# Performance work log

Measured on AMD Instinct MI355X. Metric: run time of the kernel, lower is better.

Reference implementation:

```python
import jax, jax.numpy as jnp
import numpy as np
import math

B, S, D = 4, 2048, 768
H = 12
DH = D // H  # 64
NEG = -1e10

def setup_inputs() -> dict:
    key = jax.random.key(0)
    ks = jax.random.split(key, 8)
    scale = 0.02
    return {
        "hidden_states": jax.random.normal(ks[0], (B, S, D), dtype=jnp.float32),
        "attention_mask": jnp.zeros((B, 1, 1, S), dtype=jnp.float32),
        "Wq": jax.random.normal(ks[1], (D, D), dtype=jnp.float32) * scale,
        "bq": jnp.zeros((D,), dtype=jnp.float32),
        "Wk": jax.random.normal(ks[2], (D, D), dtype=jnp.float32) * scale,
        "bk": jnp.zeros((D,), dtype=jnp.float32),
        "Wv": jax.random.normal(ks[3], (D, D), dtype=jnp.float32) * scale,
        "bv": jnp.zeros((D,), dtype=jnp.float32),
    }

def reference(hidden_states, attention_mask, Wq, bq, Wk, bk, Wv, bv):
    # Linear projections; note attention_mask is accepted but unused, matching the torch module.
    def split_heads(x):  # [B,S,D] -> [B,H,S,DH]
        return x.reshape(B, S, H, DH).transpose(0, 2, 1, 3)
    q = split_heads(hidden_states @ Wq + bq)
    k = split_heads(hidden_states @ Wk + bk)
    v = split_heads(hidden_states @ Wv + bv)
    scores = jnp.einsum("bhqd,bhkd->bhqk", q, k) / math.sqrt(DH)
    causal = jnp.tril(jnp.ones((S, S), dtype=bool))  # masked_fill(mask==0, -1e10)
    scores = jnp.where(causal, scores, NEG)
    probs = jax.nn.softmax(scores, axis=-1)
    # dropout prob = 0.0 (eval) -> identity
    ctx = jnp.einsum("bhqk,bhkd->bhqd", probs, v)
    return ctx.transpose(0, 2, 1, 3).reshape(B, S, D)
```

## Files before the change

kernel.cpp:

```cpp
#include <hip/hip_runtime.h>
#include <hip/hip_bf16.h>

#define B_  4
#define S_  2048
#define D_  768
#define H_  12
#define DH_ 64

typedef __bf16 bf16;
typedef __attribute__((ext_vector_type(8))) __bf16 bf16x8;
typedef __attribute__((ext_vector_type(4))) __bf16 bf16x4;
typedef __attribute__((ext_vector_type(4))) float floatx4;

__device__ __forceinline__ int chunk_off(int qt) {
    if (qt < 8)  return qt;
    if (qt < 16) return 8 + 2 * (qt - 8);
    if (qt < 24) return 24 + 3 * (qt - 16);
    return 48 + 4 * (qt - 24);
}

__global__ __launch_bounds__(256) void cvt_f32_bf16(const float* __restrict__ in,
                                                    bf16* __restrict__ out, int n4) {
    int i = blockIdx.x * 256 + threadIdx.x;
    if (i < n4) {
        float4 v = ((const float4*)in)[i];
        bf16x4 o;
        o[0] = (bf16)v.x; o[1] = (bf16)v.y; o[2] = (bf16)v.z; o[3] = (bf16)v.w;
        *(bf16x4*)(out + (size_t)i * 4) = o;
    }
}

__global__ __launch_bounds__(256) void w_transpose(const float* __restrict__ w0,
                                                   const float* __restrict__ w1,
                                                   const float* __restrict__ w2,
                                                   bf16* __restrict__ Wt)
{
    const int which = blockIdx.z;
    const float* W = (which == 0) ? w0 : (which == 1 ? w1 : w2);
    bf16* dst = Wt + (size_t)which * D_ * D_;
    __shared__ bf16 t[64 * 72];
    const int k0 = blockIdx.x * 64, n0 = blockIdx.y * 64;
    const int tid = threadIdx.x;
    {
        int r = tid >> 2;
        int c0 = (tid & 3) * 16;
        #pragma unroll
        for (int q = 0; q < 4; q++) {
            float4 v = *(const float4*)(W + (size_t)(k0 + r) * D_ + n0 + c0 + q * 4);
            t[(c0 + q * 4 + 0) * 72 + r] = (bf16)v.x;
            t[(c0 + q * 4 + 1) * 72 + r] = (bf16)v.y;
            t[(c0 + q * 4 + 2) * 72 + r] = (bf16)v.z;
            t[(c0 + q * 4 + 3) * 72 + r] = (bf16)v.w;
        }
    }
    __syncthreads();
    {
        int n = tid >> 3, seg = tid & 7;
        *(bf16x8*)(dst + (size_t)(n0 + n) * D_ + k0 + seg * 8) =
            *(const bf16x8*)(t + n * 72 + seg * 8);
        *(bf16x8*)(dst + (size_t)(n0 + n + 32) * D_ + k0 + seg * 8) =
            *(const bf16x8*)(t + (n + 32) * 72 + seg * 8);
    }
}

__global__ __launch_bounds__(256) void qkv_gemm(
    const bf16* __restrict__ Xb, const bf16* __restrict__ Wt,
    const float* __restrict__ bq, const float* __restrict__ bk,
    const float* __restrict__ bv, bf16* __restrict__ QKV)
{
    const int which = blockIdx.z;
    const bf16* Wm = Wt + (size_t)which * D_ * D_;
    const float* bias = (which == 0) ? bq : (which == 1 ? bk : bv);
    bf16* out = QKV + (size_t)which * B_ * H_ * S_ * DH_;

    __shared__ bf16 As[128 * 72];
    __shared__ bf16 Bs[128 * 72];

    const int tid  = threadIdx.x;
    const int wave = tid >> 6, lane = tid & 63;
    const int wr = wave >> 1, wc = wave & 1;
    const int g = lane >> 4, ln = lane & 15;
    const int m0 = blockIdx.x * 128, n0 = blockIdx.y * 128;

    floatx4 acc[4][4];
    #pragma unroll
    for (int i = 0; i < 4; i++)
        #pragma unroll
        for (int j = 0; j < 4; j++)
            acc[i][j] = (floatx4){0.f, 0.f, 0.f, 0.f};

    int row_[4], seg_[4];
    #pragma unroll
    for (int t = 0; t < 4; t++) { int fc = tid + t * 256; row_[t] = fc >> 3; seg_[t] = fc & 7; }

    bf16x8 apf[4], bpf[4];
    #pragma unroll
    for (int t = 0; t < 4; t++) {
        apf[t] = *(const bf16x8*)(Xb + (size_t)(m0 + row_[t]) * D_ + seg_[t] * 8);
        bpf[t] = *(const bf16x8*)(Wm + (size_t)(n0 + row_[t]) * D_ + seg_[t] * 8);
    }

    for (int k0 = 0; k0 < D_; k0 += 64) {
        __syncthreads();
        #pragma unroll
        for (int t = 0; t < 4; t++) {
            *(bf16x8*)(As + row_[t] * 72 + seg_[t] * 8) = apf[t];
            *(bf16x8*)(Bs + row_[t] * 72 + seg_[t] * 8) = bpf[t];
        }
        __syncthreads();
        if (k0 + 64 < D_) {
            #pragma unroll
            for (int t = 0; t < 4; t++) {
                apf[t] = *(const bf16x8*)(Xb + (size_t)(m0 + row_[t]) * D_ + k0 + 64 + seg_[t] * 8);
                bpf[t] = *(const bf16x8*)(Wm + (size_t)(n0 + row_[t]) * D_ + k0 + 64 + seg_[t] * 8);
            }
        }
        #pragma unroll
        for (int ks = 0; ks < 2; ks++) {
            bf16x8 af[4], bfr[4];
            #pragma unroll
            for (int i = 0; i < 4; i++)
                af[i] = *(const bf16x8*)(As + (wr * 64 + i * 16 + ln) * 72 + ks * 32 + g * 8);
            #pragma unroll
            for (int j = 0; j < 4; j++)
                bfr[j] = *(const bf16x8*)(Bs + (wc * 64 + j * 16 + ln) * 72 + ks * 32 + g * 8);
            #pragma unroll
            for (int i = 0; i < 4; i++)
                #pragma unroll
                for (int j = 0; j < 4; j++)
                    acc[i][j] = __builtin_amdgcn_mfma_f32_16x16x32_bf16(af[i], bfr[j], acc[i][j], 0, 0, 0);
        }
    }

    #pragma unroll
    for (int i = 0; i < 4; i++) {
        #pragma unroll
        for (int j = 0; j < 4; j++) {
            int col = n0 + wc * 64 + j * 16 + ln;
            float bv_ = bias[col];
            int h = col >> 6, dh = col & 63;
            int rowbase = m0 + wr * 64 + i * 16 + g * 4;
            int b = rowbase >> 11, s0 = rowbase & 2047;
            if (which == 2) {
                bf16x4 o;
                #pragma unroll
                for (int r = 0; r < 4; r++) o[r] = (bf16)(acc[i][j][r] + bv_);
                *(bf16x4*)(out + ((size_t)((b * H_ + h) * DH_ + dh)) * S_ + s0) = o;
            } else {
                #pragma unroll
                for (int r = 0; r < 4; r++)
                    out[(((size_t)(b * H_ + h) * S_ + s0 + r) << 6) + dh] =
                        (bf16)(acc[i][j][r] + bv_);
            }
        }
    }
}

__global__ __launch_bounds__(256) void attn_chunk(const bf16* __restrict__ QKV,
                                                  float* __restrict__ out,
                                                  bf16* __restrict__ Opart,
                                                  float* __restrict__ Lpart)
{
    const int cid = 79 - blockIdx.x;
    const int bh = blockIdx.y;
    const int b = bh / H_, h = bh % H_;

    int qt, c;
    if (cid < 8)       { qt = cid; c = 0; }
    else if (cid < 24) { qt = 8 + ((cid - 8) >> 1); c = (cid - 8) & 1; }
    else if (cid < 48) { int t3 = cid - 24; qt = 16 + t3 / 3; c = t3 - (qt - 16) * 3; }
    else               { int t4 = cid - 48; qt = 24 + (t4 >> 2); c = t4 & 3; }
    const int nch = (qt >> 3) + 1;
    const int kt0 = c * 8;
    const int kt1 = min(kt0 + 7, qt);

    const size_t MAT = (size_t)B_ * H_ * S_ * DH_;
    const bf16* Q  = QKV +           (size_t)bh * S_ * DH_;
    const bf16* K  = QKV + MAT +     (size_t)bh * S_ * DH_;
    const bf16* Vt = QKV + 2 * MAT + (size_t)bh * S_ * DH_;

    __shared__ bf16 Ks[64 * 72];
    __shared__ bf16 Vts[64 * 72];
    __shared__ bf16 Ps[4][16 * 72];

    const int tid  = threadIdx.x;
    const int wave = tid >> 6, lane = tid & 63;
    const int g = lane >> 4, ln = lane & 15;
    const int srow = tid >> 3, sseg = tid & 7;

    bf16x8 qf[2];
    {
        const bf16* qrow = Q + (size_t)(qt * 64 + wave * 16 + ln) * DH_;
        qf[0] = *(const bf16x8*)(qrow + g * 8);
        qf[1] = *(const bf16x8*)(qrow + 32 + g * 8);
    }

    bf16x8 ones;
    #pragma unroll
    for (int i = 0; i < 8; i++) ones[i] = (bf16)1.0f;

    floatx4 accO[4];
    #pragma unroll
    for (int j = 0; j < 4; j++) accO[j] = (floatx4){0.f, 0.f, 0.f, 0.f};
    floatx4 accL = (floatx4){0.f, 0.f, 0.f, 0.f};

    const bf16* kptr = K  + (size_t)(kt0 * 64 + srow) * DH_ + sseg * 8;
    const bf16* vptr = Vt + (size_t)srow * S_ + kt0 * 64 + sseg * 8;

    bf16x8 ka = *(const bf16x8*)kptr;
    bf16x8 kb = *(const bf16x8*)(kptr + 32 * DH_);
    bf16x8 va = *(const bf16x8*)vptr;
    bf16x8 vb = *(const bf16x8*)(vptr + (size_t)32 * S_);

    for (int kt = kt0; kt <= kt1; ++kt) {
        __syncthreads();
        *(bf16x8*)(Ks  + srow * 72 + sseg * 8) = ka;
        *(bf16x8*)(Ks  + (srow + 32) * 72 + sseg * 8) = kb;
        *(bf16x8*)(Vts + srow * 72 + sseg * 8) = va;
        *(bf16x8*)(Vts + (srow + 32) * 72 + sseg * 8) = vb;
        __syncthreads();
        if (kt < kt1) {
            kptr += 64 * DH_;
            vptr += 64;
            ka = *(const bf16x8*)kptr;
            kb = *(const bf16x8*)(kptr + 32 * DH_);
            va = *(const bf16x8*)vptr;
            vb = *(const bf16x8*)(vptr + (size_t)32 * S_);
        }

        floatx4 accS[4];
        #pragma unroll
        for (int j = 0; j < 4; j++) accS[j] = (floatx4){0.f, 0.f, 0.f, 0.f};
        #pragma unroll
        for (int j = 0; j < 4; j++) {
            #pragma unroll
            for (int cc = 0; cc < 2; cc++) {
                bf16x8 kf = *(const bf16x8*)(Ks + (j * 16 + ln) * 72 + cc * 32 + g * 8);
                accS[j] = __builtin_amdgcn_mfma_f32_16x16x32_bf16(qf[cc], kf, accS[j], 0, 0, 0);
            }
        }

        #pragma unroll
        for (int j = 0; j < 4; j++)
            #pragma unroll
            for (int r = 0; r < 4; r++)
                accS[j][r] = __expf(accS[j][r] * 0.125f);
        if (kt == qt) {
            #pragma unroll
            for (int j = 0; j < 4; j++) {
                int krow = j * 16 + ln;
                #pragma unroll
                for (int r = 0; r < 4; r++) {
                    int qrow = wave * 16 + g * 4 + r;
                    if (krow > qrow) accS[j][r] = 0.f;
                }
            }
        }

        bf16* Pw = Ps[wave];
        #pragma unroll
        for (int j = 0; j < 4; j++)
            #pragma unroll
            for (int r = 0; r < 4; r++)
                Pw[(g * 4 + r) * 72 + j * 16 + ln] = (bf16)accS[j][r];

        #pragma unroll
        for (int cc = 0; cc < 2; cc++) {
            bf16x8 pf = *(const bf16x8*)(Pw + ln * 72 + cc * 32 + g * 8);
            accL = __builtin_amdgcn_mfma_f32_16x16x32_bf16(pf, ones, accL, 0, 0, 0);
            #pragma unroll
            for (int j = 0; j < 4; j++) {
                bf16x8 vf = *(const bf16x8*)(Vts + (j * 16 + ln) * 72 + cc * 32 + g * 8);
                accO[j] = __builtin_amdgcn_mfma_f32_16x16x32_bf16(pf, vf, accO[j], 0, 0, 0);
            }
        }
    }

    if (nch == 1) {
        float inv[4];
        #pragma unroll
        for (int r = 0; r < 4; r++) inv[r] = 1.0f / accL[r];
        #pragma unroll
        for (int j = 0; j < 4; j++) {
            int dh = j * 16 + ln;
            #pragma unroll
            for (int r = 0; r < 4; r++) {
                int q = qt * 64 + wave * 16 + g * 4 + r;
                out[((size_t)(b * S_ + q)) * D_ + h * DH_ + dh] = accO[j][r] * inv[r];
            }
        }
    } else {
        const int chunk = bh * 80 + chunk_off(qt) + c;
        bf16x8 p0, p1;
        #pragma unroll
        for (int e = 0; e < 8; e++) {
            p0[e] = (bf16)accO[e >> 2][e & 3];
            p1[e] = (bf16)accO[2 + (e >> 2)][e & 3];
        }
        bf16* dst = Opart + (size_t)chunk * 4096 + tid * 16;
        *(bf16x8*)dst = p0;
        *(bf16x8*)(dst + 8) = p1;
        if (ln == 0) {
            #pragma unroll
            for (int r = 0; r < 4; r++)
                Lpart[chunk * 64 + wave * 16 + g * 4 + r] = accL[r];
        }
    }
}

__global__ __launch_bounds__(256) void attn_reduce(const bf16* __restrict__ Opart,
                                                   const float* __restrict__ Lpart,
                                                   float* __restrict__ out)
{
    const int qt = 8 + blockIdx.x;
    const int bh = blockIdx.y;
    const int b = bh / H_, h = bh % H_;
    const int nch = (qt >> 3) + 1;
    const int cb = bh * 80 + chunk_off(qt);

    const int tid  = threadIdx.x;
    const int wave = tid >> 6, lane = tid & 63;
    const int g = lane >> 4, ln = lane & 15;

    float o[16];
    #pragma unroll
    for (int e = 0; e < 16; e++) o[e] = 0.f;
    float ls[4] = {0.f, 0.f, 0.f, 0.f};

    for (int cidx = 0; cidx < nch; cidx++) {
        const bf16* p = Opart + (size_t)(cb + cidx) * 4096 + tid * 16;
        bf16x8 v0 = *(const bf16x8*)p;
        bf16x8 v1 = *(const bf16x8*)(p + 8);
        #pragma unroll
        for (int e = 0; e < 8; e++) { o[e] += (float)v0[e]; o[8 + e] += (float)v1[e]; }
        #pragma unroll
        for (int r = 0; r < 4; r++)
            ls[r] += Lpart[(cb + cidx) * 64 + wave * 16 + g * 4 + r];
    }
    float inv[4];
    #pragma unroll
    for (int r = 0; r < 4; r++) inv[r] = 1.0f / ls[r];
    #pragma unroll
    for (int j = 0; j < 4; j++) {
        int dh = j * 16 + ln;
        #pragma unroll
        for (int r = 0; r < 4; r++) {
            int q = qt * 64 + wave * 16 + g * 4 + r;
            out[((size_t)(b * S_ + q)) * D_ + h * DH_ + dh] = o[j * 4 + r] * inv[r];
        }
    }
}

extern "C" void kernel_launch(void* const* d_in, const int* in_sizes, int n_in,
                              void* d_out, int out_size, void* d_ws, size_t ws_size,
                              hipStream_t stream) {
    const float* hs = (const float*)d_in[0];
    const float* Wq = (const float*)d_in[2];
    const float* bq = (const float*)d_in[3];
    const float* Wk = (const float*)d_in[4];
    const float* bk = (const float*)d_in[5];
    const float* Wv = (const float*)d_in[6];
    const float* bv = (const float*)d_in[7];
    float* out = (float*)d_out;

    bf16* Xb    = (bf16*)d_ws;
    bf16* Wt    = Xb + (size_t)8192 * 768;
    bf16* QKV   = Wt + (size_t)3 * 768 * 768;
    bf16* Opart = QKV + (size_t)3 * B_ * H_ * S_ * DH_;
    float* Lpart = (float*)(Opart + (size_t)3840 * 4096);

    cvt_f32_bf16<<<6144, 256, 0, stream>>>(hs, Xb, 1572864);
    w_transpose<<<dim3(12, 12, 3), 256, 0, stream>>>(Wq, Wk, Wv, Wt);
    qkv_gemm<<<dim3(64, 6, 3), 256, 0, stream>>>(Xb, Wt, bq, bk, bv, QKV);
    attn_chunk<<<dim3(80, 48), 256, 0, stream>>>(QKV, out, Opart, Lpart);
    attn_reduce<<<dim3(24, 48), 256, 0, stream>>>(Opart, Lpart, out);
}
```

Baseline: 202.1 us.

## Process two query tiles per attention block and transpose P via shuffles

```diff
diff --git a/kernel.cpp b/kernel.cpp
--- a/kernel.cpp
+++ b/kernel.cpp
@@ -12,11 +12,17 @@
 typedef __attribute__((ext_vector_type(4))) __bf16 bf16x4;
 typedef __attribute__((ext_vector_type(4))) float floatx4;
 
-__device__ __forceinline__ int chunk_off(int qt) {
-    if (qt < 8)  return qt;
-    if (qt < 16) return 8 + 2 * (qt - 8);
-    if (qt < 24) return 24 + 3 * (qt - 16);
-    return 48 + 4 * (qt - 24);
+__device__ __forceinline__ int chunk_off2(int qt2) {
+    if (qt2 < 4)  return qt2;
+    if (qt2 < 8)  return 4 + 2 * (qt2 - 4);
+    if (qt2 < 12) return 12 + 3 * (qt2 - 8);
+    return 24 + 4 * (qt2 - 12);
+}
+
+__device__ __forceinline__ unsigned pack_bf16(float a, float b) {
+    unsigned short ua = __builtin_bit_cast(unsigned short, (bf16)a);
+    unsigned short ub = __builtin_bit_cast(unsigned short, (bf16)b);
+    return (unsigned)ua | ((unsigned)ub << 16);
 }
 
 __global__ __launch_bounds__(256) void cvt_f32_bf16(const float* __restrict__ in,
@@ -132,6 +138,7 @@
         }
     }
 
+    const float sc = (which == 0) ? 0.125f : 1.0f;
     #pragma unroll
     for (int i = 0; i < 4; i++) {
         #pragma unroll
@@ -150,7 +157,7 @@
                 #pragma unroll
                 for (int r = 0; r < 4; r++)
                     out[(((size_t)(b * H_ + h) * S_ + s0 + r) << 6) + dh] =
-                        (bf16)(acc[i][j][r] + bv_);
+                        (bf16)((acc[i][j][r] + bv_) * sc);
             }
         }
     }
@@ -161,18 +168,18 @@
                                                   bf16* __restrict__ Opart,
                                                   float* __restrict__ Lpart)
 {
-    const int cid = 79 - blockIdx.x;
+    const int cid = 39 - blockIdx.x;
     const int bh = blockIdx.y;
     const int b = bh / H_, h = bh % H_;
 
-    int qt, c;
-    if (cid < 8)       { qt = cid; c = 0; }
-    else if (cid < 24) { qt = 8 + ((cid - 8) >> 1); c = (cid - 8) & 1; }
-    else if (cid < 48) { int t3 = cid - 24; qt = 16 + t3 / 3; c = t3 - (qt - 16) * 3; }
-    else               { int t4 = cid - 48; qt = 24 + (t4 >> 2); c = t4 & 3; }
-    const int nch = (qt >> 3) + 1;
+    int qt2, c;
+    if (cid < 4)       { qt2 = cid; c = 0; }
+    else if (cid < 12) { int t = cid - 4;  qt2 = 4 + (t >> 1);  c = t & 1; }
+    else if (cid < 24) { int t = cid - 12; qt2 = 8 + t / 3;     c = t - 3 * (t / 3); }
+    else               { int t = cid - 24; qt2 = 12 + (t >> 2); c = t & 3; }
+    const int nch = (2 * qt2 + 9) >> 3;
     const int kt0 = c * 8;
-    const int kt1 = min(kt0 + 7, qt);
+    const int kt1 = min(kt0 + 7, 2 * qt2 + 1);
 
     const size_t MAT = (size_t)B_ * H_ * S_ * DH_;
     const bf16* Q  = QKV +           (size_t)bh * S_ * DH_;
@@ -181,36 +188,41 @@
 
     __shared__ bf16 Ks[64 * 72];
     __shared__ bf16 Vts[64 * 72];
-    __shared__ bf16 Ps[4][16 * 72];
 
     const int tid  = threadIdx.x;
     const int wave = tid >> 6, lane = tid & 63;
     const int g = lane >> 4, ln = lane & 15;
     const int srow = tid >> 3, sseg = tid & 7;
-
-    bf16x8 qf[2];
-    {
-        const bf16* qrow = Q + (size_t)(qt * 64 + wave * 16 + ln) * DH_;
-        qf[0] = *(const bf16x8*)(qrow + g * 8);
-        qf[1] = *(const bf16x8*)(qrow + 32 + g * 8);
+    const int qbase = qt2 * 128;
+
+    bf16x8 qf[2][2];
+    #pragma unroll
+    for (int t = 0; t < 2; t++) {
+        const bf16* qrow = Q + (size_t)(qbase + t * 64 + wave * 16 + ln) * DH_;
+        qf[t][0] = *(const bf16x8*)(qrow + g * 8);
+        qf[t][1] = *(const bf16x8*)(qrow + 32 + g * 8);
     }
 
     bf16x8 ones;
     #pragma unroll
     for (int i = 0; i < 8; i++) ones[i] = (bf16)1.0f;
 
-    floatx4 accO[4];
-    #pragma unroll
-    for (int j = 0; j < 4; j++) accO[j] = (floatx4){0.f, 0.f, 0.f, 0.f};
-    floatx4 accL = (floatx4){0.f, 0.f, 0.f, 0.f};
+    floatx4 accO[2][4];
+    #pragma unroll
+    for (int t = 0; t < 2; t++)
+        #pragma unroll
+        for (int j = 0; j < 4; j++) accO[t][j] = (floatx4){0.f, 0.f, 0.f, 0.f};
+    floatx4 accL[2] = {(floatx4){0.f, 0.f, 0.f, 0.f}, (floatx4){0.f, 0.f, 0.f, 0.f}};
 
     const bf16* kptr = K  + (size_t)(kt0 * 64 + srow) * DH_ + sseg * 8;
     const bf16* vptr = Vt + (size_t)srow * S_ + kt0 * 64 + sseg * 8;
-
     bf16x8 ka = *(const bf16x8*)kptr;
     bf16x8 kb = *(const bf16x8*)(kptr + 32 * DH_);
     bf16x8 va = *(const bf16x8*)vptr;
     bf16x8 vb = *(const bf16x8*)(vptr + (size_t)32 * S_);
+
+    const int s0lane = ((lane >> 4) & 1) * 32 + ln;
+    const bool hi = (lane >= 32);
 
     for (int kt = kt0; kt <= kt1; ++kt) {
         __syncthreads();
@@ -228,82 +240,108 @@
             vb = *(const bf16x8*)(vptr + (size_t)32 * S_);
         }
 
-        floatx4 accS[4];
-        #pragma unroll
-        for (int j = 0; j < 4; j++) accS[j] = (floatx4){0.f, 0.f, 0.f, 0.f};
-        #pragma unroll
-        for (int j = 0; j < 4; j++) {
-            #pragma unroll
-            for (int cc = 0; cc < 2; cc++) {
-                bf16x8 kf = *(const bf16x8*)(Ks + (j * 16 + ln) * 72 + cc * 32 + g * 8);
-                accS[j] = __builtin_amdgcn_mfma_f32_16x16x32_bf16(qf[cc], kf, accS[j], 0, 0, 0);
-            }
-        }
-
+        bf16x8 kf[4][2];
         #pragma unroll
         for (int j = 0; j < 4; j++)
             #pragma unroll
-            for (int r = 0; r < 4; r++)
-                accS[j][r] = __expf(accS[j][r] * 0.125f);
-        if (kt == qt) {
+            for (int cc = 0; cc < 2; cc++)
+                kf[j][cc] = *(const bf16x8*)(Ks + (j * 16 + ln) * 72 + cc * 32 + g * 8);
+
+        floatx4 accS[2][4];
+        #pragma unroll
+        for (int t = 0; t < 2; t++)
+            #pragma unroll
+            for (int j = 0; j < 4; j++) accS[t][j] = (floatx4){0.f, 0.f, 0.f, 0.f};
+        #pragma unroll
+        for (int t = 0; t < 2; t++)
+            #pragma unroll
+            for (int j = 0; j < 4; j++)
+                #pragma unroll
+                for (int cc = 0; cc < 2; cc++)
+                    accS[t][j] = __builtin_amdgcn_mfma_f32_16x16x32_bf16(
+                        kf[j][cc], qf[t][cc], accS[t][j], 0, 0, 0);
+
+        unsigned pd0[2][4], pd1[2][4];
+        #pragma unroll
+        for (int t = 0; t < 2; t++) {
+            const int qg = qbase + t * 64 + wave * 16 + ln;
+            const bool domask = (kt >= 2 * qt2 + t);
             #pragma unroll
             for (int j = 0; j < 4; j++) {
-                int krow = j * 16 + ln;
+                float p[4];
                 #pragma unroll
                 for (int r = 0; r < 4; r++) {
-                    int qrow = wave * 16 + g * 4 + r;
-                    if (krow > qrow) accS[j][r] = 0.f;
+                    p[r] = __expf(accS[t][j][r]);
+                    if (domask) {
+                        int key = kt * 64 + j * 16 + g * 4 + r;
+                        if (key > qg) p[r] = 0.f;
+                    }
                 }
-            }
-        }
-
-        bf16* Pw = Ps[wave];
-        #pragma unroll
-        for (int j = 0; j < 4; j++)
-            #pragma unroll
-            for (int r = 0; r < 4; r++)
-                Pw[(g * 4 + r) * 72 + j * 16 + ln] = (bf16)accS[j][r];
+                pd0[t][j] = pack_bf16(p[0], p[1]);
+                pd1[t][j] = pack_bf16(p[2], p[3]);
+            }
+        }
 
         #pragma unroll
         for (int cc = 0; cc < 2; cc++) {
-            bf16x8 pf = *(const bf16x8*)(Pw + ln * 72 + cc * 32 + g * 8);
-            accL = __builtin_amdgcn_mfma_f32_16x16x32_bf16(pf, ones, accL, 0, 0, 0);
+            bf16x8 ptf[2];
+            #pragma unroll
+            for (int t = 0; t < 2; t++) {
+                unsigned a0 = __shfl(pd0[t][2 * cc],     s0lane);
+                unsigned b0 = __shfl(pd0[t][2 * cc + 1], s0lane);
+                unsigned a1 = __shfl(pd1[t][2 * cc],     s0lane);
+                unsigned b1 = __shfl(pd1[t][2 * cc + 1], s0lane);
+                unsigned a2 = __shfl(pd0[t][2 * cc],     s0lane + 16);
+                unsigned b2 = __shfl(pd0[t][2 * cc + 1], s0lane + 16);
+                unsigned a3 = __shfl(pd1[t][2 * cc],     s0lane + 16);
+                unsigned b3 = __shfl(pd1[t][2 * cc + 1], s0lane + 16);
+                uint4 w;
+                w.x = hi ? b0 : a0;
+                w.y = hi ? b1 : a1;
+                w.z = hi ? b2 : a2;
+                w.w = hi ? b3 : a3;
+                ptf[t] = __builtin_bit_cast(bf16x8, w);
+                accL[t] = __builtin_amdgcn_mfma_f32_16x16x32_bf16(ones, ptf[t], accL[t], 0, 0, 0);
+            }
             #pragma unroll
             for (int j = 0; j < 4; j++) {
                 bf16x8 vf = *(const bf16x8*)(Vts + (j * 16 + ln) * 72 + cc * 32 + g * 8);
-                accO[j] = __builtin_amdgcn_mfma_f32_16x16x32_bf16(pf, vf, accO[j], 0, 0, 0);
+                #pragma unroll
+                for (int t = 0; t < 2; t++)
+                    accO[t][j] = __builtin_amdgcn_mfma_f32_16x16x32_bf16(
+                        vf, ptf[t], accO[t][j], 0, 0, 0);
             }
         }
     }
 
     if (nch == 1) {
-        float inv[4];
-        #pragma unroll
-        for (int r = 0; r < 4; r++) inv[r] = 1.0f / accL[r];
-        #pragma unroll
-        for (int j = 0; j < 4; j++) {
-            int dh = j * 16 + ln;
-            #pragma unroll
-            for (int r = 0; r < 4; r++) {
-                int q = qt * 64 + wave * 16 + g * 4 + r;
-                out[((size_t)(b * S_ + q)) * D_ + h * DH_ + dh] = accO[j][r] * inv[r];
+        #pragma unroll
+        for (int t = 0; t < 2; t++) {
+            float inv = 1.0f / accL[t][0];
+            int q = qbase + t * 64 + wave * 16 + ln;
+            float* orow = out + (size_t)(b * S_ + q) * D_ + h * DH_;
+            #pragma unroll
+            for (int j = 0; j < 4; j++) {
+                float4 o;
+                o.x = accO[t][j][0] * inv; o.y = accO[t][j][1] * inv;
+                o.z = accO[t][j][2] * inv; o.w = accO[t][j][3] * inv;
+                *(float4*)(orow + j * 16 + g * 4) = o;
             }
         }
     } else {
-        const int chunk = bh * 80 + chunk_off(qt) + c;
-        bf16x8 p0, p1;
-        #pragma unroll
-        for (int e = 0; e < 8; e++) {
-            p0[e] = (bf16)accO[e >> 2][e & 3];
-            p1[e] = (bf16)accO[2 + (e >> 2)][e & 3];
-        }
-        bf16* dst = Opart + (size_t)chunk * 4096 + tid * 16;
-        *(bf16x8*)dst = p0;
-        *(bf16x8*)(dst + 8) = p1;
-        if (ln == 0) {
-            #pragma unroll
-            for (int r = 0; r < 4; r++)
-                Lpart[chunk * 64 + wave * 16 + g * 4 + r] = accL[r];
+        const int chunk = bh * 40 + chunk_off2(qt2) + c;
+        bf16* obase = Opart + (size_t)chunk * 8192;
+        #pragma unroll
+        for (int t = 0; t < 2; t++) {
+            int ql = t * 64 + wave * 16 + ln;
+            #pragma unroll
+            for (int j = 0; j < 4; j++) {
+                bf16x4 o;
+                #pragma unroll
+                for (int r = 0; r < 4; r++) o[r] = (bf16)accO[t][j][r];
+                *(bf16x4*)(obase + ql * 64 + j * 16 + g * 4) = o;
+            }
+            if (g == 0) Lpart[chunk * 128 + ql] = accL[t][0];
         }
     }
 }
@@ -312,42 +350,38 @@
                                                    const float* __restrict__ Lpart,
                                                    float* __restrict__ out)
 {
-    const int qt = 8 + blockIdx.x;
+    const int qt2 = 4 + blockIdx.x;
     const int bh = blockIdx.y;
     const int b = bh / H_, h = bh % H_;
-    const int nch = (qt >> 3) + 1;
-    const int cb = bh * 80 + chunk_off(qt);
-
-    const int tid  = threadIdx.x;
-    const int wave = tid >> 6, lane = tid & 63;
-    const int g = lane >> 4, ln = lane & 15;
-
-    float o[16];
-    #pragma unroll
-    for (int e = 0; e < 16; e++) o[e] = 0.f;
-    float ls[4] = {0.f, 0.f, 0.f, 0.f};
+    const int nch = (2 * qt2 + 9) >> 3;
+    const int cb = bh * 40 + chunk_off2(qt2);
+
+    const int e = threadIdx.x;
+    const int ql = e >> 1, dh0 = (e & 1) * 32;
+
+    float o[32];
+    #pragma unroll
+    for (int i = 0; i < 32; i++) o[i] = 0.f;
+    float l = 0.f;
 
     for (int cidx = 0; cidx < nch; cidx++) {
-        const bf16* p = Opart + (size_t)(cb + cidx) * 4096 + tid * 16;
-        bf16x8 v0 = *(const bf16x8*)p;
-        bf16x8 v1 = *(const bf16x8*)(p + 8);
-        #pragma unroll
-        for (int e = 0; e < 8; e++) { o[e] += (float)v0[e]; o[8 + e] += (float)v1[e]; }
-        #pragma unroll
-        for (int r = 0; r < 4; r++)
-            ls[r] += Lpart[(cb + cidx) * 64 + wave * 16 + g * 4 + r];
-    }
-    float inv[4];
-    #pragma unroll
-    for (int r = 0; r < 4; r++) inv[r] = 1.0f / ls[r];
-    #pragma unroll
-    for (int j = 0; j < 4; j++) {
-        int dh = j * 16 + ln;
-        #pragma unroll
-        for (int r = 0; r < 4; r++) {
-            int q = qt * 64 + wave * 16 + g * 4 + r;
-            out[((size_t)(b * S_ + q)) * D_ + h * DH_ + dh] = o[j * 4 + r] * inv[r];
-        }
+        const bf16* p = Opart + (size_t)(cb + cidx) * 8192 + ql * 64 + dh0;
+        #pragma unroll
+        for (int m = 0; m < 4; m++) {
+            bf16x8 v = *(const bf16x8*)(p + m * 8);
+            #pragma unroll
+            for (int k = 0; k < 8; k++) o[m * 8 + k] += (float)v[k];
+        }
+        l += Lpart[(cb + cidx) * 128 + ql];
+    }
+    float inv = 1.0f / l;
+    float* orow = out + (size_t)(b * S_ + qt2 * 128 + ql) * D_ + h * DH_ + dh0;
+    #pragma unroll
+    for (int m = 0; m < 8; m++) {
+        float4 v;
+        v.x = o[m * 4 + 0] * inv; v.y = o[m * 4 + 1] * inv;
+        v.z = o[m * 4 + 2] * inv; v.w = o[m * 4 + 3] * inv;
+        *(float4*)(orow + m * 4) = v;
     }
 }
 
@@ -367,11 +401,11 @@
     bf16* Wt    = Xb + (size_t)8192 * 768;
     bf16* QKV   = Wt + (size_t)3 * 768 * 768;
     bf16* Opart = QKV + (size_t)3 * B_ * H_ * S_ * DH_;
-    float* Lpart = (float*)(Opart + (size_t)3840 * 4096);
+    float* Lpart = (float*)(Opart + (size_t)1920 * 8192);
 
     cvt_f32_bf16<<<6144, 256, 0, stream>>>(hs, Xb, 1572864);
     w_transpose<<<dim3(12, 12, 3), 256, 0, stream>>>(Wq, Wk, Wv, Wt);
     qkv_gemm<<<dim3(64, 6, 3), 256, 0, stream>>>(Xb, Wt, bq, bk, bv, QKV);
-    attn_chunk<<<dim3(80, 48), 256, 0, stream>>>(QKV, out, Opart, Lpart);
-    attn_reduce<<<dim3(24, 48), 256, 0, stream>>>(Opart, Lpart, out);
-}
+    attn_chunk<<<dim3(40, 48), 256, 0, stream>>>(QKV, out, Opart, Lpart);
+    attn_reduce<<<dim3(12, 48), 256, 0, stream>>>(Opart, Lpart, out);
+}
```

New measurement: 210.5 us. 1.04x slower.
